# Kernel tuning notes

Measured on AMD Instinct MI355X. Metric: run time of the kernel, lower is better.

Reference implementation:

```python
import jax, jax.numpy as jnp
import numpy as np

B, N, DIM = 8, 8192, 256
K, CDIM = 4096, 1024
COMMIT = 0.25


def setup_inputs() -> dict:
    key = jax.random.key(0)
    ks = jax.random.split(key, 4)
    x = jax.random.normal(ks[0], (B, N, DIM), dtype=jnp.float32)
    ln_g = jnp.ones((DIM,), jnp.float32)
    ln_b = jnp.zeros((DIM,), jnp.float32)
    w_pre = jax.random.normal(ks[1], (DIM, CDIM), jnp.float32) / np.sqrt(DIM)
    b_pre = jnp.zeros((CDIM,), jnp.float32)
    embed = jax.random.normal(ks[2], (K, CDIM), jnp.float32)
    w_post = jax.random.normal(ks[3], (CDIM, DIM), jnp.float32) / np.sqrt(CDIM)
    b_post = jnp.zeros((DIM,), jnp.float32)
    return {"x": x, "ln_g": ln_g, "ln_b": ln_b, "w_pre": w_pre, "b_pre": b_pre,
            "embed": embed, "w_post": w_post, "b_post": b_post}


def reference(x, ln_g, ln_b, w_pre, b_pre, embed, w_post, b_post):
    # LayerNorm over last dim (eps=1e-5, torch default)
    mu = jnp.mean(x, axis=-1, keepdims=True)
    var = jnp.mean((x - mu) ** 2, axis=-1, keepdims=True)
    xn = (x - mu) * jax.lax.rsqrt(var + 1e-5) * ln_g + ln_b
    # GELU (exact, erf-based as in torch default) then Linear dim->codebook_dim
    z_e = jax.nn.gelu(xn, approximate=False) @ w_pre + b_pre  # (B,N,CDIM)
    flat = z_e.reshape(-1, CDIM)                              # (B*N, CDIM)
    # squared euclidean distances to codebook, argmin, gather
    z_sq = jnp.sum(flat * flat, axis=1, keepdims=True)        # (BN,1)
    e_sq = jnp.sum(embed * embed, axis=1)                     # (K,)
    dist = z_sq - 2.0 * (flat @ embed.T) + e_sq[None, :]      # (BN,K)
    indices = jnp.argmin(dist, axis=1)                        # (BN,)
    z_q = embed[indices]                                      # (BN,CDIM)
    # commitment loss (z_q detached)
    commit = COMMIT * jnp.mean((flat - jax.lax.stop_gradient(z_q)) ** 2)
    # straight-through estimator
    z_q_st = flat + jax.lax.stop_gradient(z_q - flat)
    z_q_st = z_q_st.reshape(B, N, CDIM)
    quantized = z_q_st @ w_post + b_post                      # (B,N,DIM)
    return quantized, indices.reshape(B, N), commit
```

## Files before the change

### kernel.cpp

```cpp
#include <hip/hip_runtime.h>

#define BN_ROWS 65536
#define DIMX 256
#define CDIM 1024
#define KCODES 4096
#define NSP 16
#define NSLOT 5
#define NENT 6
#define CMARG 12.0f
#define RMARG 12.0f
#define QS 24.0f
#define INV_S2 (1.0f / (QS * QS))
#define FLT_BIG 3.402823466e+38f

static const size_t OFF_ESQ   = 0;
static const size_t OFF_IDXF  = 16384;
static const size_t OFF_CROW  = 278528;
static const size_t OFF_EPOST = 540672;
static const size_t OFF_EI8   = 4734976;
static const size_t OFF_NFLAG = 8929280;
static const size_t OFF_FLAG  = 8929344;
static const size_t OFF_CAND  = 9191488;

typedef __attribute__((ext_vector_type(4))) int i32x4;

#define GLOAD_LDS16(gsrc, ldst)                                                \
  __builtin_amdgcn_global_load_lds(                                            \
      (const __attribute__((address_space(1))) void*)(gsrc),                   \
      (__attribute__((address_space(3))) void*)(ldst), 16, 0, 0)

__device__ inline char q8(float f) {
  return (char)__float2int_rn(fminf(fmaxf(f * QS, -127.f), 127.f));
}
__device__ inline unsigned fkey(float s) {
  unsigned b = __float_as_uint(s);
  return b ^ ((unsigned)((int)b >> 31) | 0x80000000u);
}
__device__ inline float keyinv(unsigned k) {
  unsigned b = (k & 0x80000000u) ? (k ^ 0x80000000u) : ~k;
  return __uint_as_float(b);
}

__global__ __launch_bounds__(256) void k_esq(const float* __restrict__ embed,
                                             float* __restrict__ e_sq) {
  const int t = threadIdx.x, wv = t >> 6, lane = t & 63;
  const int row = blockIdx.x * 4 + wv;
  const float* e = embed + (size_t)row * CDIM;
  float s = 0.f;
  for (int k = lane * 4; k < CDIM; k += 256) {
    float4 v = *(const float4*)(e + k);
    s = fmaf(v.x, v.x, s); s = fmaf(v.y, v.y, s);
    s = fmaf(v.z, v.z, s); s = fmaf(v.w, v.w, s);
  }
#pragma unroll
  for (int o = 32; o > 0; o >>= 1) s += __shfl_xor(s, o);
  if (lane == 0) e_sq[row] = s;
}

__global__ __launch_bounds__(256) void k_ei8(const float* __restrict__ embed,
                                             char* __restrict__ Ei8) {
  const int t = threadIdx.x;
  const size_t row = blockIdx.x;
  float4 v = *(const float4*)(embed + row * CDIM + t * 4);
  *(char4*)(Ei8 + row * CDIM + t * 4) =
      make_char4(q8(v.x), q8(v.y), q8(v.z), q8(v.w));
}

__global__ __launch_bounds__(256) void k_ln_gelu_gemm(
    const float* __restrict__ x, const float* __restrict__ ln_g,
    const float* __restrict__ ln_b, const float* __restrict__ w_pre,
    const float* __restrict__ b_pre, float* __restrict__ zf,
    char* __restrict__ zi8, int row0) {
  __shared__ float g[16][DIMX];
  const int t = threadIdx.x;
  const int lrow0 = blockIdx.x * 16;
  const int grow0 = row0 + lrow0;
  const int wv = t >> 6, lane = t & 63;
#pragma unroll
  for (int j = 0; j < 4; ++j) {
    const int r = wv * 4 + j;
    const float* xr = x + (size_t)(grow0 + r) * DIMX;
    float4 v = *(const float4*)(xr + lane * 4);
    float s = v.x + v.y + v.z + v.w;
    float ss = v.x * v.x + v.y * v.y + v.z * v.z + v.w * v.w;
#pragma unroll
    for (int o = 32; o > 0; o >>= 1) { s += __shfl_xor(s, o); ss += __shfl_xor(ss, o); }
    const float mu = s * (1.0f / 256.0f);
    const float var = ss * (1.0f / 256.0f) - mu * mu;
    const float rstd = rsqrtf(var + 1e-5f);
    float vv[4] = {v.x, v.y, v.z, v.w};
#pragma unroll
    for (int q = 0; q < 4; ++q) {
      const int d = lane * 4 + q;
      float xn = (vv[q] - mu) * rstd * ln_g[d] + ln_b[d];
      g[r][d] = 0.5f * xn * (1.0f + erff(xn * 0.70710678118654752f));
    }
  }
  __syncthreads();
  float acc[16][4];
#pragma unroll
  for (int r = 0; r < 16; ++r)
#pragma unroll
    for (int c = 0; c < 4; ++c) acc[r][c] = 0.f;
#pragma unroll 2
  for (int d0 = 0; d0 < DIMX; d0 += 4) {
    float4 w0 = *(const float4*)(w_pre + (size_t)(d0 + 0) * CDIM + t * 4);
    float4 w1 = *(const float4*)(w_pre + (size_t)(d0 + 1) * CDIM + t * 4);
    float4 w2 = *(const float4*)(w_pre + (size_t)(d0 + 2) * CDIM + t * 4);
    float4 w3 = *(const float4*)(w_pre + (size_t)(d0 + 3) * CDIM + t * 4);
#pragma unroll
    for (int r = 0; r < 16; ++r) {
      float4 gv = *(const float4*)&g[r][d0];
      acc[r][0] = fmaf(gv.x, w0.x, acc[r][0]);
      acc[r][1] = fmaf(gv.x, w0.y, acc[r][1]);
      acc[r][2] = fmaf(gv.x, w0.z, acc[r][2]);
      acc[r][3] = fmaf(gv.x, w0.w, acc[r][3]);
      acc[r][0] = fmaf(gv.y, w1.x, acc[r][0]);
      acc[r][1] = fmaf(gv.y, w1.y, acc[r][1]);
      acc[r][2] = fmaf(gv.y, w1.z, acc[r][2]);
      acc[r][3] = fmaf(gv.y, w1.w, acc[r][3]);
      acc[r][0] = fmaf(gv.z, w2.x, acc[r][0]);
      acc[r][1] = fmaf(gv.z, w2.y, acc[r][1]);
      acc[r][2] = fmaf(gv.z, w2.z, acc[r][2]);
      acc[r][3] = fmaf(gv.z, w2.w, acc[r][3]);
      acc[r][0] = fmaf(gv.w, w3.x, acc[r][0]);
      acc[r][1] = fmaf(gv.w, w3.y, acc[r][1]);
      acc[r][2] = fmaf(gv.w, w3.z, acc[r][2]);
      acc[r][3] = fmaf(gv.w, w3.w, acc[r][3]);
    }
  }
  float4 bp = *(const float4*)(b_pre + t * 4);
#pragma unroll
  for (int r = 0; r < 16; ++r) {
    float4 o;
    o.x = acc[r][0] + bp.x; o.y = acc[r][1] + bp.y;
    o.z = acc[r][2] + bp.z; o.w = acc[r][3] + bp.w;
    *(float4*)(zf + (size_t)(lrow0 + r) * CDIM + t * 4) = o;
    *(char4*)(zi8 + (size_t)(lrow0 + r) * CDIM + t * 4) =
        make_char4(q8(o.x), q8(o.y), q8(o.z), q8(o.w));
  }
}

__global__ __launch_bounds__(512) void k_score(
    const char* __restrict__ Ei8, const char* __restrict__ Zi8,
    const float* __restrict__ e_sq, uint2* __restrict__ cand, int chunk) {
  __shared__ __align__(16) char lds[2][32768];
  const int t = threadIdx.x;
  const int cpx = gridDim.x >> 3;
  const int bx = (blockIdx.x & 7) * cpx + (blockIdx.x >> 3);
  const int zblk = bx / NSP, csp = bx % NSP;
  const int wid = t >> 6, l = t & 63;
  const int wr = wid >> 2, wc = wid & 3;
  const int lg = l >> 4, lo16 = l & 15;
  const int rowbase = zblk * 256;
  const int m0 = csp * 256;
  const int wr8 = wr * 8, wc4 = wc * 4, l16 = l * 16;

  const bool isA = (wid < 4);
  const int q = wid & 3;
  const char* sarr = isA ? Ei8 : Zi8;
  const int sbase = isA ? m0 : rowbase;
  const char* sp0 = sarr + (size_t)(sbase + q * 64 + lo16) * 1024 + lg * 16;
  const int dstbase = (isA ? 0 : 16384) + q * 4096;

  i32x4 acc[8][4];
#pragma unroll
  for (int mi = 0; mi < 8; ++mi)
#pragma unroll
    for (int ni = 0; ni < 4; ++ni) acc[mi][ni] = (i32x4){0, 0, 0, 0};

  {
    char* D = &lds[0][dstbase];
#pragma unroll
    for (int u = 0; u < 4; ++u) GLOAD_LDS16(sp0 + u * 16384, D + u * 1024);
  }

  for (int kt = 0; kt < 16; ++kt) {
    const char* Lc = lds[kt & 1];
    asm volatile("s_waitcnt vmcnt(0)" ::: "memory");
    __builtin_amdgcn_s_barrier();
    __builtin_amdgcn_sched_barrier(0);
    if (kt < 15) {
      char* Dst = &lds[(kt + 1) & 1][dstbase];
      const char* spk = sp0 + (kt + 1) * 64;
#pragma unroll
      for (int u = 0; u < 4; ++u) GLOAD_LDS16(spk + u * 16384, Dst + u * 1024);
    }
    i32x4 bh[4], a[8];
#pragma unroll
    for (int ni = 0; ni < 4; ++ni)
      bh[ni] = *(const i32x4*)(Lc + 16384 + (wc4 + ni) * 1024 + l16);
#pragma unroll
    for (int u = 0; u < 8; ++u)
      a[u] = *(const i32x4*)(Lc + (wr8 + u) * 1024 + l16);
    asm volatile("s_waitcnt lgkmcnt(0)" ::: "memory");
    __builtin_amdgcn_sched_barrier(0);
    __builtin_amdgcn_s_setprio(1);
#pragma unroll
    for (int u = 0; u < 8; ++u)
#pragma unroll
      for (int ni = 0; ni < 4; ++ni)
        acc[u][ni] = __builtin_amdgcn_mfma_i32_16x16x64_i8(a[u], bh[ni],
                                                           acc[u][ni], 0, 0, 0);
    __builtin_amdgcn_s_setprio(0);
  }

  float s1[4];
  int i1[4];
#pragma unroll
  for (int i = 0; i < 4; ++i) { s1[i] = FLT_BIG; i1[i] = 0x7fffffff; }
#pragma unroll
  for (int mi = 0; mi < 8; ++mi) {
    const int c0 = m0 + wr * 128 + mi * 16 + lg * 4;
    float4 es = *(const float4*)(e_sq + c0);
    float esv[4] = {es.x, es.y, es.z, es.w};
#pragma unroll
    for (int ni = 0; ni < 4; ++ni) {
#pragma unroll
      for (int j = 0; j < 4; ++j) {
        const float s = fmaf(-2.0f * INV_S2, (float)acc[mi][ni][j], esv[j]);
        const int c = c0 + j;
        if (s < s1[ni] || (s == s1[ni] && c < i1[ni])) { s1[ni] = s; i1[ni] = c; }
      }
    }
  }

  unsigned long long* red = (unsigned long long*)&lds[0][0];
  float* sb = (float*)&lds[0][4096];
  unsigned* sbi = (unsigned*)&lds[0][5120];
  unsigned* cnt = (unsigned*)&lds[0][6144];
  uint2* slot = (uint2*)&lds[0][7168];

  __syncthreads();
#pragma unroll
  for (int ni = 0; ni < 4; ++ni) {
    unsigned long long k1v =
        (((unsigned long long)fkey(s1[ni])) << 32) | (unsigned)i1[ni];
    unsigned long long o1 = __shfl_xor(k1v, 16);
    k1v = o1 < k1v ? o1 : k1v;
    o1 = __shfl_xor(k1v, 32);
    k1v = o1 < k1v ? o1 : k1v;
    if (lg == 0) {
      const int r = wc * 64 + ni * 16 + lo16;
      red[r * 2 + wr] = k1v;
    }
  }
  __syncthreads();
  if (t < 256) {
    unsigned long long a1 = red[t * 2 + 0], b1 = red[t * 2 + 1];
    if (b1 < a1) a1 = b1;
    sb[t] = keyinv((unsigned)(a1 >> 32));
    sbi[t] = (unsigned)(a1 & 0xFFFFFFFFull);
    cnt[t] = 0;
  }
  __syncthreads();
#pragma unroll
  for (int mi = 0; mi < 8; ++mi) {
    const int c0 = m0 + wr * 128 + mi * 16 + lg * 4;
    float4 es = *(const float4*)(e_sq + c0);
    float esv[4] = {es.x, es.y, es.z, es.w};
#pragma unroll
    for (int ni = 0; ni < 4; ++ni) {
      const int r = wc * 64 + ni * 16 + lo16;
      const float thr = sb[r] + CMARG;
#pragma unroll
      for (int j = 0; j < 4; ++j) {
        const float s = fmaf(-2.0f * INV_S2, (float)acc[mi][ni][j], esv[j]);
        const unsigned c = (unsigned)(c0 + j);
        if (s < thr && c != sbi[r]) {
          unsigned pos = atomicAdd(&cnt[r], 1u);
          if (pos < NSLOT)
            slot[r * NSLOT + pos] = make_uint2(__float_as_uint(s), c);
        }
      }
    }
  }
  __syncthreads();
  if (t < 256) {
    uint2* g = cand + (size_t)(rowbase + t) * (NSP * NENT) + csp * NENT;
    const unsigned ov = (cnt[t] > NSLOT) ? 0x40000000u : 0u;
    g[0] = make_uint2(__float_as_uint(sb[t]), sbi[t] | ov);
    const unsigned n = cnt[t] > NSLOT ? NSLOT : cnt[t];
#pragma unroll
    for (int k = 0; k < NSLOT; ++k)
      g[1 + k] = (k < (int)n) ? slot[t * NSLOT + k]
                              : make_uint2(__float_as_uint(FLT_BIG), 0xFFFFFFFFu);
  }
}

__global__ __launch_bounds__(256) void k_refine(
    const uint2* __restrict__ cand, const float* __restrict__ zf,
    const float* __restrict__ embed, int* __restrict__ idxf,
    float* __restrict__ crow, float* __restrict__ out_idx,
    int* __restrict__ flag_rows, int* __restrict__ nflag, int chunk,
    int row0) {
  const int t = threadIdx.x, wid = t >> 6, l = t & 63;
  const int lrow = blockIdx.x * 4 + wid;
  if (lrow >= chunk) return;
  const int grow = row0 + lrow;
  const uint2* base = cand + (size_t)lrow * (NSP * NENT);
  const uint2 e0 = base[l];
  const uint2 e1 = (l < 32) ? base[64 + l]
                            : make_uint2(__float_as_uint(FLT_BIG), 0xFFFFFFFFu);
  const bool is0 = (l % NENT) == 0;
  const bool is1 = (l < 32) && (((64 + l) % NENT) == 0);
  float gm = FLT_BIG;
  if (is0) gm = fminf(gm, __uint_as_float(e0.x));
  if (is1) gm = fminf(gm, __uint_as_float(e1.x));
#pragma unroll
  for (int o = 32; o > 0; o >>= 1) gm = fminf(gm, __shfl_xor(gm, o));
  const float thr = gm + RMARG;
  bool myovf = (is0 && (e0.y & 0x40000000u) && __uint_as_float(e0.x) < thr) ||
               (is1 && (e1.y & 0x40000000u) && __uint_as_float(e1.x) < thr);
  const bool ovf = __any(myovf);

  float zv[16];
#pragma unroll
  for (int j = 0; j < 16; ++j) zv[j] = zf[(size_t)lrow * CDIM + l + 64 * j];

  double d1 = 1e300;
  int i1 = 0x7fffffff;
#define PROC(E)                                                                \
  {                                                                            \
    const float sc_ = __uint_as_float(E.x);                                    \
    const int id_ = (int)(E.y & 0xFFFFu);                                      \
    unsigned long long mask = __ballot(sc_ < thr && id_ < KCODES);             \
    while (mask) {                                                             \
      const int src = __ffsll((unsigned long long)mask) - 1;                   \
      mask &= mask - 1;                                                        \
      const int c = __shfl(id_, src);                                          \
      const float* e = embed + (size_t)c * CDIM;                               \
      double dd = 0.0;                                                         \
      _Pragma("unroll") for (int j = 0; j < 16; ++j) {                         \
        const double df = (double)zv[j] - (double)e[l + 64 * j];               \
        dd = fma(df, df, dd);                                                  \
      }                                                                        \
      _Pragma("unroll") for (int o = 32; o > 0; o >>= 1) dd +=                 \
          __shfl_xor(dd, o);                                                   \
      if (dd < d1 || (dd == d1 && c < i1)) { d1 = dd; i1 = c; }                \
    }                                                                          \
  }
  PROC(e0);
  PROC(e1);
#undef PROC
  if (l == 0) {
    idxf[grow] = i1;
    out_idx[grow] = (float)i1;
    crow[grow] = (float)d1;
    if (ovf) {
      const int s = atomicAdd(nflag, 1);
      flag_rows[s] = lrow;
    }
  }
}

__global__ __launch_bounds__(256) void k_exact(
    const float* __restrict__ zf, const float* __restrict__ embed,
    const int* __restrict__ flag_rows, const int* __restrict__ nflag,
    int* __restrict__ idxf, float* __restrict__ crow,
    float* __restrict__ out_idx, int row0) {
  __shared__ double wd[4];
  __shared__ int wcidx[4];
  const int t = threadIdx.x;
  const int wid = t >> 6, l = t & 63;
  const int n = *nflag;

  for (int fi = blockIdx.x; fi < n; fi += gridDim.x) {
    const int lrow = flag_rows[fi];
    const int grow = row0 + lrow;
    float zr[16];
#pragma unroll
    for (int j = 0; j < 16; ++j) zr[j] = zf[(size_t)lrow * CDIM + l + 64 * j];
    double dmin = 1e300;
    int cmin = 0x7fffffff;
    for (int ci = 0; ci < 1024; ++ci) {
      const int c = wid * 1024 + ci;
      const float* e = embed + (size_t)c * CDIM;
      double dd = 0.0;
#pragma unroll
      for (int j = 0; j < 16; ++j) {
        const double df = (double)zr[j] - (double)e[l + 64 * j];
        dd = fma(df, df, dd);
      }
#pragma unroll
      for (int o = 32; o > 0; o >>= 1) dd += __shfl_xor(dd, o);
      if (dd < dmin) { dmin = dd; cmin = c; }
    }
    if (l == 0) { wd[wid] = dmin; wcidx[wid] = cmin; }
    __syncthreads();
    if (t == 0) {
      double dm = wd[0]; int cm = wcidx[0];
#pragma unroll
      for (int wv = 1; wv < 4; ++wv) {
        if (wd[wv] < dm || (wd[wv] == dm && wcidx[wv] < cm)) {
          dm = wd[wv]; cm = wcidx[wv];
        }
      }
      idxf[grow] = cm;
      out_idx[grow] = (float)cm;
      crow[grow] = (float)dm;
    }
    __syncthreads();
  }
}

__global__ __launch_bounds__(256) void k_epost(const float* __restrict__ E,
                                               const float* __restrict__ w_post,
                                               float* __restrict__ E_post) {
  __shared__ float es[16][128];
  const int t = threadIdx.x;
  const int r0 = blockIdx.x * 16;
  float acc[16];
#pragma unroll
  for (int r = 0; r < 16; ++r) acc[r] = 0.f;
  for (int k0 = 0; k0 < CDIM; k0 += 128) {
    __syncthreads();
#pragma unroll
    for (int p = 0; p < 2; ++p) {
      const int fl = (p * 256 + t) * 4;
      const int r = fl >> 7, kk = fl & 127;
      float4 v = *(const float4*)(E + (size_t)(r0 + r) * CDIM + k0 + kk);
      *(float4*)&es[r][kk] = v;
    }
    __syncthreads();
#pragma unroll 4
    for (int d = 0; d < 128; ++d) {
      const float w = w_post[(size_t)(k0 + d) * DIMX + t];
#pragma unroll
      for (int r = 0; r < 16; ++r) acc[r] = fmaf(es[r][d], w, acc[r]);
    }
  }
#pragma unroll
  for (int r = 0; r < 16; ++r)
    E_post[(size_t)(r0 + r) * DIMX + t] = acc[r];
}

__global__ __launch_bounds__(256) void k_gather(const float* __restrict__ E_post,
                                                const int* __restrict__ idx,
                                                const float* __restrict__ b_post,
                                                float* __restrict__ outq) {
  const int t = threadIdx.x;
  const int r0 = blockIdx.x * 16;
  const float bp = b_post[t];
#pragma unroll
  for (int i = 0; i < 16; ++i) {
    const int row = r0 + i;
    outq[(size_t)row * DIMX + t] = E_post[(size_t)idx[row] * DIMX + t] + bp;
  }
}

__global__ __launch_bounds__(256) void k_commit_final(
    const float* __restrict__ crow, float* __restrict__ out_commit) {
  const int t = threadIdx.x;
  double s = 0.0;
  for (int i = t; i < BN_ROWS; i += 256) s += (double)crow[i];
#pragma unroll
  for (int o = 32; o > 0; o >>= 1) s += __shfl_xor(s, o);
  __shared__ double wsum[4];
  if ((t & 63) == 0) wsum[t >> 6] = s;
  __syncthreads();
  if (t == 0)
    *out_commit = (float)(0.25 * (wsum[0] + wsum[1] + wsum[2] + wsum[3]) /
                          (65536.0 * 1024.0));
}

extern "C" void kernel_launch(void* const* d_in, const int* in_sizes, int n_in,
                              void* d_out, int out_size, void* d_ws,
                              size_t ws_size, hipStream_t stream) {
  const float* x = (const float*)d_in[0];
  const float* ln_g = (const float*)d_in[1];
  const float* ln_b = (const float*)d_in[2];
  const float* w_pre = (const float*)d_in[3];
  const float* b_pre = (const float*)d_in[4];
  const float* embed = (const float*)d_in[5];
  const float* w_post = (const float*)d_in[6];
  const float* b_post = (const float*)d_in[7];

  float* out = (float*)d_out;
  float* outq = out;
  float* out_idx = out + 16777216;
  float* out_commit = out + 16842752;

  char* ws = (char*)d_ws;
  float* e_sq = (float*)(ws + OFF_ESQ);
  int* idxf = (int*)(ws + OFF_IDXF);
  float* crow = (float*)(ws + OFF_CROW);
  float* E_post = (float*)(ws + OFF_EPOST);
  char* Ei8 = (char*)(ws + OFF_EI8);
  int* nflag = (int*)(ws + OFF_NFLAG);
  int* flag_rows = (int*)(ws + OFF_FLAG);

  int chunk = 4096;
  while (chunk < BN_ROWS &&
         OFF_CAND + (size_t)(chunk * 2) * 5888ull <= ws_size)
    chunk *= 2;
  uint2* cand = (uint2*)(ws + OFF_CAND);
  char* zi8 = ws + OFF_CAND + (size_t)chunk * 768;
  float* zf = (float*)(ws + OFF_CAND + (size_t)chunk * 768 +
                       (size_t)chunk * 1024);

  k_esq<<<KCODES / 4, 256, 0, stream>>>(embed, e_sq);
  k_ei8<<<KCODES, 256, 0, stream>>>(embed, Ei8);
  k_epost<<<KCODES / 16, 256, 0, stream>>>(embed, w_post, E_post);

  for (int row0 = 0; row0 < BN_ROWS; row0 += chunk) {
    hipMemsetAsync(nflag, 0, sizeof(int), stream);
    k_ln_gelu_gemm<<<chunk / 16, 256, 0, stream>>>(x, ln_g, ln_b, w_pre, b_pre,
                                                   zf, zi8, row0);
    k_score<<<(chunk / 256) * NSP, 512, 0, stream>>>(Ei8, zi8, e_sq, cand,
                                                     chunk);
    k_refine<<<chunk / 4, 256, 0, stream>>>(cand, zf, embed, idxf, crow,
                                            out_idx, flag_rows, nflag, chunk,
                                            row0);
    k_exact<<<128, 256, 0, stream>>>(zf, embed, flag_rows, nflag, idxf, crow,
                                     out_idx, row0);
  }

  k_gather<<<BN_ROWS / 16, 256, 0, stream>>>(E_post, idxf, b_post, outq);
  k_commit_final<<<1, 256, 0, stream>>>(crow, out_commit);
}
```

Baseline: 1.331 ms.

## Pre-pack int8 operands in MFMA fragment layout and load directly to registers

The int8 codebook and z quantization kernels now write their outputs in a blocked layout where each 1 KiB block holds exactly one MFMA 16x64 fragment per lane. The scoring kernel drops its LDS double-buffered staging with barriers and instead has each wave load its A and B fragments straight from global memory into registers, with the k-loop fully unrolled. This removes LDS traffic and block-wide synchronisation, and shrinks LDS so more blocks can be resident. The cost is that operand reuse now depends on L1/L2, since every wave refetches shared fragments from global memory with no explicit prefetch.

```diff
diff --git a/kernel.cpp b/kernel.cpp
--- a/kernel.cpp
+++ b/kernel.cpp
@@ -22,12 +22,8 @@
 static const size_t OFF_FLAG  = 8929344;
 static const size_t OFF_CAND  = 9191488;
 
+
 typedef __attribute__((ext_vector_type(4))) int i32x4;
-
-#define GLOAD_LDS16(gsrc, ldst)                                                \
-  __builtin_amdgcn_global_load_lds(                                            \
-      (const __attribute__((address_space(1))) void*)(gsrc),                   \
-      (__attribute__((address_space(3))) void*)(ldst), 16, 0, 0)
 
 __device__ inline char q8(float f) {
   return (char)__float2int_rn(fminf(fmaxf(f * QS, -127.f), 127.f));
@@ -58,11 +54,14 @@
 }
 
 __global__ __launch_bounds__(256) void k_ei8(const float* __restrict__ embed,
-                                             char* __restrict__ Ei8) {
-  const int t = threadIdx.x;
-  const size_t row = blockIdx.x;
-  float4 v = *(const float4*)(embed + row * CDIM + t * 4);
-  *(char4*)(Ei8 + row * CDIM + t * 4) =
+                                             char* __restrict__ PA) {
+  const int t = threadIdx.x;
+  const int c = blockIdx.x;
+  float4 v = *(const float4*)(embed + (size_t)c * CDIM + t * 4);
+  const int k = t * 4;
+  const size_t blk = (size_t)(c >> 4) * 16 + (k >> 6);
+  const int lane = ((k >> 4) & 3) * 16 + (c & 15);
+  *(char4*)(PA + blk * 1024 + lane * 16 + (k & 15)) =
       make_char4(q8(v.x), q8(v.y), q8(v.z), q8(v.w));
 }
 
@@ -130,21 +129,25 @@
     }
   }
   float4 bp = *(const float4*)(b_pre + t * 4);
+  const int k = t * 4;
+  const size_t pblk0 = (size_t)(lrow0 >> 4) * 16 + (k >> 6);
+  const int plane_k = ((k >> 4) & 3) * 16;
+  const int pbyte = k & 15;
 #pragma unroll
   for (int r = 0; r < 16; ++r) {
     float4 o;
     o.x = acc[r][0] + bp.x; o.y = acc[r][1] + bp.y;
     o.z = acc[r][2] + bp.z; o.w = acc[r][3] + bp.w;
     *(float4*)(zf + (size_t)(lrow0 + r) * CDIM + t * 4) = o;
-    *(char4*)(zi8 + (size_t)(lrow0 + r) * CDIM + t * 4) =
+    *(char4*)(zi8 + pblk0 * 1024 + (plane_k + r) * 16 + pbyte) =
         make_char4(q8(o.x), q8(o.y), q8(o.z), q8(o.w));
   }
 }
 
 __global__ __launch_bounds__(512) void k_score(
-    const char* __restrict__ Ei8, const char* __restrict__ Zi8,
+    const char* __restrict__ PA, const char* __restrict__ PB,
     const float* __restrict__ e_sq, uint2* __restrict__ cand, int chunk) {
-  __shared__ __align__(16) char lds[2][32768];
+  __shared__ __align__(16) char lds[18432];
   const int t = threadIdx.x;
   const int cpx = gridDim.x >> 3;
   const int bx = (blockIdx.x & 7) * cpx + (blockIdx.x >> 3);
@@ -154,14 +157,11 @@
   const int lg = l >> 4, lo16 = l & 15;
   const int rowbase = zblk * 256;
   const int m0 = csp * 256;
-  const int wr8 = wr * 8, wc4 = wc * 4, l16 = l * 16;
-
-  const bool isA = (wid < 4);
-  const int q = wid & 3;
-  const char* sarr = isA ? Ei8 : Zi8;
-  const int sbase = isA ? m0 : rowbase;
-  const char* sp0 = sarr + (size_t)(sbase + q * 64 + lo16) * 1024 + lg * 16;
-  const int dstbase = (isA ? 0 : 16384) + q * 4096;
+
+  const char* pa0 =
+      PA + ((size_t)((m0 >> 4) + wr * 8) * 16) * 1024 + l * 16;
+  const char* pb0 =
+      PB + ((size_t)((rowbase >> 4) + wc * 4) * 16) * 1024 + l * 16;
 
   i32x4 acc[8][4];
 #pragma unroll
@@ -169,40 +169,21 @@
 #pragma unroll
     for (int ni = 0; ni < 4; ++ni) acc[mi][ni] = (i32x4){0, 0, 0, 0};
 
-  {
-    char* D = &lds[0][dstbase];
-#pragma unroll
-    for (int u = 0; u < 4; ++u) GLOAD_LDS16(sp0 + u * 16384, D + u * 1024);
-  }
-
+#pragma unroll
   for (int kt = 0; kt < 16; ++kt) {
-    const char* Lc = lds[kt & 1];
-    asm volatile("s_waitcnt vmcnt(0)" ::: "memory");
-    __builtin_amdgcn_s_barrier();
-    __builtin_amdgcn_sched_barrier(0);
-    if (kt < 15) {
-      char* Dst = &lds[(kt + 1) & 1][dstbase];
-      const char* spk = sp0 + (kt + 1) * 64;
-#pragma unroll
-      for (int u = 0; u < 4; ++u) GLOAD_LDS16(spk + u * 16384, Dst + u * 1024);
-    }
-    i32x4 bh[4], a[8];
+    i32x4 a[8], b[4];
+#pragma unroll
+    for (int u = 0; u < 8; ++u)
+      a[u] = *(const i32x4*)(pa0 + u * 16384 + kt * 1024);
 #pragma unroll
     for (int ni = 0; ni < 4; ++ni)
-      bh[ni] = *(const i32x4*)(Lc + 16384 + (wc4 + ni) * 1024 + l16);
+      b[ni] = *(const i32x4*)(pb0 + ni * 16384 + kt * 1024);
 #pragma unroll
     for (int u = 0; u < 8; ++u)
-      a[u] = *(const i32x4*)(Lc + (wr8 + u) * 1024 + l16);
-    asm volatile("s_waitcnt lgkmcnt(0)" ::: "memory");
-    __builtin_amdgcn_sched_barrier(0);
-    __builtin_amdgcn_s_setprio(1);
-#pragma unroll
-    for (int u = 0; u < 8; ++u)
 #pragma unroll
       for (int ni = 0; ni < 4; ++ni)
-        acc[u][ni] = __builtin_amdgcn_mfma_i32_16x16x64_i8(a[u], bh[ni],
+        acc[u][ni] = __builtin_amdgcn_mfma_i32_16x16x64_i8(a[u], b[ni],
                                                            acc[u][ni], 0, 0, 0);
-    __builtin_amdgcn_s_setprio(0);
   }
 
   float s1[4];
@@ -225,11 +206,11 @@
     }
   }
 
-  unsigned long long* red = (unsigned long long*)&lds[0][0];
-  float* sb = (float*)&lds[0][4096];
-  unsigned* sbi = (unsigned*)&lds[0][5120];
-  unsigned* cnt = (unsigned*)&lds[0][6144];
-  uint2* slot = (uint2*)&lds[0][7168];
+  unsigned long long* red = (unsigned long long*)&lds[0];
+  float* sb = (float*)&lds[4096];
+  unsigned* sbi = (unsigned*)&lds[5120];
+  unsigned* cnt = (unsigned*)&lds[6144];
+  uint2* slot = (uint2*)&lds[7168];
 
   __syncthreads();
 #pragma unroll
```

Result: slower. 1.561 ms (+17.3%).
